# Kernel optimization log

Measured on AMD Instinct MI355X. Metric: run time of the kernel, lower is better.

The kernel has to match this reference:

```python
import jax, jax.numpy as jnp
import numpy as np

B, X_DIM, Z_DIM, K = 16384, 784, 64, 64
LOG2PI = 1.8378770664093453


def setup_inputs() -> dict:
    key = jax.random.key(0)
    ks = jax.random.split(key, 8)
    pi_raw = jax.random.uniform(ks[1], (B, K), dtype=jnp.float32) + 1e-3
    pi = pi_raw / jnp.sum(pi_raw, axis=1, keepdims=True)
    return {
        "x": jax.random.normal(ks[0], (B, X_DIM), dtype=jnp.float32),
        "pi": pi,
        "qz_mu": jax.random.normal(ks[2], (B, Z_DIM), dtype=jnp.float32),
        "qz_logsigma": 0.5 * jax.random.normal(ks[3], (B, Z_DIM), dtype=jnp.float32),
        "eps": jax.random.normal(ks[4], (B, Z_DIM), dtype=jnp.float32),
        "pz_y_mu": jax.random.normal(ks[5], (K, Z_DIM), dtype=jnp.float32),
        "pz_y_logsigma": jnp.zeros((K, Z_DIM), dtype=jnp.float32),  # log(init_sigma=1.0)
        "W_dec": jax.random.normal(ks[6], (Z_DIM, X_DIM), dtype=jnp.float32) / np.sqrt(Z_DIM),
        "b_dec": jnp.zeros((X_DIM,), dtype=jnp.float32),
    }


def reference(x, pi, qz_mu, qz_logsigma, eps, pz_y_mu, pz_y_logsigma, W_dec, b_dec):
    # GMMVAE.elbo with num_samples=1; rsample reparameterized with fixed eps.
    qs = jnp.exp(qz_logsigma)                      # [B, z]
    z = qz_mu + qs * eps                           # [B, z]

    # log p(x | z): unit-variance Gaussian likelihood with linear decoder
    mean = z @ W_dec + b_dec                       # [B, x]
    log_px_z = jnp.sum(-0.5 * (x - mean) ** 2 - 0.5 * LOG2PI)

    # py_z: vectorized over all k components (fuses the original Python loop)
    ps = jnp.exp(pz_y_logsigma)                    # [k, z]
    diff = z[:, None, :] - pz_y_mu[None, :, :]     # [B, k, z]
    comp_lp = jnp.sum(-0.5 * (diff / ps[None]) ** 2 - pz_y_logsigma[None] - 0.5 * LOG2PI, axis=-1)  # [B, k]
    log_pi = jnp.log(pi)
    pzy = comp_lp + log_pi                         # [B, k]
    log_py_z = pzy - jax.scipy.special.logsumexp(pzy, axis=1, keepdims=True)
    probs = jnp.exp(log_py_z)                      # [B, k]

    # kl_y = sum_b KL(Cat(py_z) || Cat(pi))
    kl_y = jnp.sum(probs * (log_py_z - log_pi))

    # kl_z = sum_b sum_k probs[b,k] * KL(N(qz_mu, qs) || N(mu_k, ps_k)).sum(z)
    mdiff = qz_mu[:, None, :] - pz_y_mu[None, :, :]  # [B, k, z]
    klz_bk = jnp.sum(
        pz_y_logsigma[None] - qz_logsigma[:, None, :]
        + (qs[:, None, :] ** 2 + mdiff ** 2) / (2.0 * ps[None] ** 2)
        - 0.5,
        axis=-1,
    )                                              # [B, k]
    kl_z = jnp.sum(probs * klz_bk)

    elbo = (log_px_z - kl_y - kl_z) / x.shape[0]
    return elbo
```

## Files before the change

kernel.cpp:

```cpp
#include <hip/hip_runtime.h>

#define NB 16384
#define XD 784
#define ZD 64
#define KK 64
#define LOG2PI_F 1.8378770664093453f

typedef __attribute__((ext_vector_type(8))) short short8;
typedef __attribute__((ext_vector_type(4))) float floatx4;


__device__ __forceinline__ float wave_sum(float x) {
    #pragma unroll
    for (int o = 32; o > 0; o >>= 1) x += __shfl_xor(x, o, 64);
    return x;
}

__device__ __forceinline__ unsigned short f2bf(float f) {
    unsigned u = __float_as_uint(f);
    unsigned r = (u + 0x7FFF + ((u >> 16) & 1)) >> 16;
    return (unsigned short)r;
}

__device__ __forceinline__ unsigned int pack2(float a, float b) {
    return (unsigned int)f2bf(a) | ((unsigned int)f2bf(b) << 16);
}

__device__ __forceinline__ short8 pack8(const float* v) {
    short8 r;
    unsigned int* p = (unsigned int*)&r;
    p[0] = pack2(v[0], v[1]);
    p[1] = pack2(v[2], v[3]);
    p[2] = pack2(v[4], v[5]);
    p[3] = pack2(v[6], v[7]);
    return r;
}

__global__ __launch_bounds__(256) void prep_kernel(
    const float* __restrict__ W, const float* __restrict__ pmu_g,
    const float* __restrict__ plog_g, unsigned short* __restrict__ Wt,
    unsigned short* __restrict__ Bi2, unsigned short* __restrict__ Bm1,
    float* __restrict__ Sk, float* __restrict__ Gk)
{
    const int tid = threadIdx.x;
    if (blockIdx.x < 196) {
        int idx = blockIdx.x * 256 + tid;
        int k = idx / XD;
        int n = idx - k * XD;
        Wt[n * ZD + k] = f2bf(W[idx]);
        return;
    }
    const int k  = tid >> 2;
    const int q  = tid & 3;
    const int v0 = q * 16;
    float s = 0.f, g = 0.f;
    unsigned int* pi2 = (unsigned int*)&Bi2[k * 64 + v0];
    unsigned int* pm1 = (unsigned int*)&Bm1[k * 64 + v0];
    #pragma unroll
    for (int i = 0; i < 4; ++i) {
        float4 mu4 = *(const float4*)&pmu_g[k * 64 + v0 + 4 * i];
        float4 lg4 = *(const float4*)&plog_g[k * 64 + v0 + 4 * i];
        float m0[4] = {mu4.x, mu4.y, mu4.z, mu4.w};
        float l0[4] = {lg4.x, lg4.y, lg4.z, lg4.w};
        float i2v[4], m1v[4];
        #pragma unroll
        for (int j = 0; j < 4; ++j) {
            float i2 = 0.5f * __expf(-2.f * l0[j]);
            i2v[j] = i2;
            m1v[j] = m0[j] * i2;
            g = fmaf(m0[j] * m0[j], i2, g);
            s += l0[j];
        }
        pi2[i * 2 + 0] = pack2(i2v[0], i2v[1]);
        pi2[i * 2 + 1] = pack2(i2v[2], i2v[3]);
        pm1[i * 2 + 0] = pack2(m1v[0], m1v[1]);
        pm1[i * 2 + 1] = pack2(m1v[2], m1v[3]);
    }
    s += __shfl_xor(s, 1, 64);
    s += __shfl_xor(s, 2, 64);
    g += __shfl_xor(g, 1, 64);
    g += __shfl_xor(g, 2, 64);
    if (q == 0) { Sk[k] = s; Gk[k] = g; }
}

__global__ __launch_bounds__(256) void fused_kernel(
    const float* __restrict__ x, const float* __restrict__ pi,
    const float* __restrict__ qmu, const float* __restrict__ qls,
    const float* __restrict__ eps,
    const unsigned short* __restrict__ Bi2, const unsigned short* __restrict__ Bm1,
    const float* __restrict__ Sk, const float* __restrict__ Gk,
    const unsigned short* __restrict__ Wt, const float* __restrict__ bd,
    float* __restrict__ dec_p, float* __restrict__ kly_p, float* __restrict__ klz_p)
{
    const int tid   = threadIdx.x;
    const int lane  = tid & 63;
    const int wid   = tid >> 6;
    const int mm    = lane & 15;
    const int quad  = lane >> 4;
    const int row0  = blockIdx.x * 16;
    const int arow  = row0 + mm;
    const int v0    = quad * 8;
    const int v1    = 32 + quad * 8;

    float mu[16], ls[16], ep[16];
    *(float4*)&mu[0]  = *(const float4*)&qmu[arow * 64 + v0];
    *(float4*)&mu[4]  = *(const float4*)&qmu[arow * 64 + v0 + 4];
    *(float4*)&mu[8]  = *(const float4*)&qmu[arow * 64 + v1];
    *(float4*)&mu[12] = *(const float4*)&qmu[arow * 64 + v1 + 4];
    *(float4*)&ls[0]  = *(const float4*)&qls[arow * 64 + v0];
    *(float4*)&ls[4]  = *(const float4*)&qls[arow * 64 + v0 + 4];
    *(float4*)&ls[8]  = *(const float4*)&qls[arow * 64 + v1];
    *(float4*)&ls[12] = *(const float4*)&qls[arow * 64 + v1 + 4];
    *(float4*)&ep[0]  = *(const float4*)&eps[arow * 64 + v0];
    *(float4*)&ep[4]  = *(const float4*)&eps[arow * 64 + v0 + 4];
    *(float4*)&ep[8]  = *(const float4*)&eps[arow * 64 + v1];
    *(float4*)&ep[12] = *(const float4*)&eps[arow * 64 + v1 + 4];

    float zf[16], ls_sum = 0.f;
    float qsv[16];
    #pragma unroll
    for (int j = 0; j < 16; ++j) {
        qsv[j] = __expf(ls[j]);
        zf[j]  = fmaf(qsv[j], ep[j], mu[j]);
        ls_sum += ls[j];
    }
    const short8 af0 = pack8(&zf[0]), af1 = pack8(&zf[8]);

    if (wid == 3) {
        float zz[16], zm[16], q2[16], qm[16];
        #pragma unroll
        for (int j = 0; j < 16; ++j) {
            zz[j] = zf[j] * zf[j];
            zm[j] = -2.f * zf[j];
            q2[j] = fmaf(mu[j], mu[j], qsv[j] * qsv[j]);
            qm[j] = -2.f * mu[j];
        }
        float sls = ls_sum;
        sls += __shfl_xor(sls, 16, 64);
        sls += __shfl_xor(sls, 32, 64);

        const short8 az2_0 = pack8(&zz[0]), az2_1 = pack8(&zz[8]);
        const short8 azm_0 = pack8(&zm[0]), azm_1 = pack8(&zm[8]);
        const short8 aq2_0 = pack8(&q2[0]), aq2_1 = pack8(&q2[8]);
        const short8 aqm_0 = pack8(&qm[0]), aqm_1 = pack8(&qm[8]);

        short8 bi[4][2], bm[4][2];
        float skv[4], gkv[4];
        #pragma unroll
        for (int t = 0; t < 4; ++t) {
            const int kc = t * 16 + mm;
            bi[t][0] = *(const short8*)&Bi2[kc * 64 + v0];
            bi[t][1] = *(const short8*)&Bi2[kc * 64 + v1];
            bm[t][0] = *(const short8*)&Bm1[kc * 64 + v0];
            bm[t][1] = *(const short8*)&Bm1[kc * 64 + v1];
            skv[t] = Sk[kc];
            gkv[t] = Gk[kc];
        }
        float pv[4][4];
        #pragma unroll
        for (int t = 0; t < 4; ++t)
            #pragma unroll
            for (int r = 0; r < 4; ++r)
                pv[t][r] = pi[(row0 + quad * 4 + r) * 64 + t * 16 + mm];

        floatx4 acc_a[4], acc_c[4];
        #pragma unroll
        for (int t = 0; t < 4; ++t) {
            floatx4 ca = {0.f, 0.f, 0.f, 0.f};
            ca = __builtin_amdgcn_mfma_f32_16x16x32_bf16(az2_0, bi[t][0], ca, 0, 0, 0);
            ca = __builtin_amdgcn_mfma_f32_16x16x32_bf16(az2_1, bi[t][1], ca, 0, 0, 0);
            ca = __builtin_amdgcn_mfma_f32_16x16x32_bf16(azm_0, bm[t][0], ca, 0, 0, 0);
            ca = __builtin_amdgcn_mfma_f32_16x16x32_bf16(azm_1, bm[t][1], ca, 0, 0, 0);
            acc_a[t] = ca;
            floatx4 cc = {0.f, 0.f, 0.f, 0.f};
            cc = __builtin_amdgcn_mfma_f32_16x16x32_bf16(aq2_0, bi[t][0], cc, 0, 0, 0);
            cc = __builtin_amdgcn_mfma_f32_16x16x32_bf16(aq2_1, bi[t][1], cc, 0, 0, 0);
            cc = __builtin_amdgcn_mfma_f32_16x16x32_bf16(aqm_0, bm[t][0], cc, 0, 0, 0);
            cc = __builtin_amdgcn_mfma_f32_16x16x32_bf16(aqm_1, bm[t][1], cc, 0, 0, 0);
            acc_c[t] = cc;
        }

        float comp[4][4], pz[4][4];
        #pragma unroll
        for (int t = 0; t < 4; ++t) {
            const float ck = -skv[t] - 32.0f * LOG2PI_F;
            #pragma unroll
            for (int r = 0; r < 4; ++r) {
                comp[t][r] = ck - (acc_a[t][r] + gkv[t]);
                pz[t][r] = comp[t][r] + __logf(pv[t][r]);
            }
        }

        float kly = 0.f, klz = 0.f;
        #pragma unroll
        for (int r = 0; r < 4; ++r) {
            float mx = fmaxf(fmaxf(pz[0][r], pz[1][r]), fmaxf(pz[2][r], pz[3][r]));
            #pragma unroll
            for (int o = 1; o <= 8; o <<= 1) mx = fmaxf(mx, __shfl_xor(mx, o, 64));
            float e[4];
            float s = 0.f;
            #pragma unroll
            for (int t = 0; t < 4; ++t) { e[t] = __expf(pz[t][r] - mx); s += e[t]; }
            #pragma unroll
            for (int o = 1; o <= 8; o <<= 1) s += __shfl_xor(s, o, 64);
            const float lse = mx + __logf(s);
            const float inv = __frcp_rn(s);
            const float sqr = __shfl(sls, quad * 4 + r, 64);
            #pragma unroll
            for (int t = 0; t < 4; ++t) {
                const float p = e[t] * inv;
                kly = fmaf(p, comp[t][r] - lse, kly);
                klz = fmaf(p, skv[t] - sqr + acc_c[t][r] + gkv[t] - 32.0f, klz);
            }
        }

        kly = wave_sum(kly);
        klz = wave_sum(klz);
        if (lane == 0) {
            kly_p[blockIdx.x] = kly;
            klz_p[blockIdx.x] = klz;
        }
    }

    const int xrow = (row0 + quad * 4) * XD;
    float xa0, xa1, xa2, xa3, bb;
    short8 w0, w1;
    {
        const int col = wid * 16 + mm;
        xa0 = x[xrow + 0 * XD + col];
        xa1 = x[xrow + 1 * XD + col];
        xa2 = x[xrow + 2 * XD + col];
        xa3 = x[xrow + 3 * XD + col];
        bb  = bd[col];
        w0  = *(const short8*)&Wt[col * 64 + v0];
        w1  = *(const short8*)&Wt[col * 64 + v1];
    }

    float accl = 0.f;
    #pragma unroll 1
    for (int t = wid; t < 49; t += 4) {
        const float cx0 = xa0, cx1 = xa1, cx2 = xa2, cx3 = xa3, cb = bb;
        const short8 cw0 = w0, cw1 = w1;
        const int tn = t + 4;
        if (tn < 49) {
            const int col = tn * 16 + mm;
            xa0 = x[xrow + 0 * XD + col];
            xa1 = x[xrow + 1 * XD + col];
            xa2 = x[xrow + 2 * XD + col];
            xa3 = x[xrow + 3 * XD + col];
            bb  = bd[col];
            w0  = *(const short8*)&Wt[col * 64 + v0];
            w1  = *(const short8*)&Wt[col * 64 + v1];
        }
        floatx4 c = {0.f, 0.f, 0.f, 0.f};
        c = __builtin_amdgcn_mfma_f32_16x16x32_bf16(af0, cw0, c, 0, 0, 0);
        c = __builtin_amdgcn_mfma_f32_16x16x32_bf16(af1, cw1, c, 0, 0, 0);
        float d0 = cx0 - (c[0] + cb);
        float d1 = cx1 - (c[1] + cb);
        float d2 = cx2 - (c[2] + cb);
        float d3 = cx3 - (c[3] + cb);
        accl = fmaf(d0, d0, accl);
        accl = fmaf(d1, d1, accl);
        accl = fmaf(d2, d2, accl);
        accl = fmaf(d3, d3, accl);
    }

    accl = wave_sum(accl);
    if (lane == 0) dec_p[blockIdx.x * 4 + wid] = -0.5f * accl;
}

__global__ __launch_bounds__(256) void finalize_kernel(
    const float* __restrict__ dec_p, const float* __restrict__ kly_p,
    const float* __restrict__ klz_p, float* __restrict__ out)
{
    __shared__ double s0[256], s1[256], s2[256];
    const int tid = threadIdx.x;
    double a0 = 0.0, a1 = 0.0, a2 = 0.0;
    #pragma unroll
    for (int i = 0; i < 16; ++i) a0 += (double)dec_p[tid + 256 * i];
    #pragma unroll
    for (int i = 0; i < 4; ++i) {
        a1 += (double)kly_p[tid + 256 * i];
        a2 += (double)klz_p[tid + 256 * i];
    }
    s0[tid] = a0; s1[tid] = a1; s2[tid] = a2;
    __syncthreads();
    #pragma unroll
    for (int off = 128; off > 0; off >>= 1) {
        if (tid < off) {
            s0[tid] += s0[tid + off];
            s1[tid] += s1[tid + off];
            s2[tid] += s2[tid + off];
        }
        __syncthreads();
    }
    if (tid == 0) {
        double lpx = s0[0] - 0.5 * 1.8378770664093453 * (double)NB * (double)XD;
        out[0] = (float)((lpx - s1[0] - s2[0]) / (double)NB);
    }
}

extern "C" void kernel_launch(void* const* d_in, const int* in_sizes, int n_in,
                              void* d_out, int out_size, void* d_ws, size_t ws_size,
                              hipStream_t stream) {
    const float* x    = (const float*)d_in[0];
    const float* pi   = (const float*)d_in[1];
    const float* qmu  = (const float*)d_in[2];
    const float* qls  = (const float*)d_in[3];
    const float* eps  = (const float*)d_in[4];
    const float* pmu  = (const float*)d_in[5];
    const float* plog = (const float*)d_in[6];
    const float* W    = (const float*)d_in[7];
    const float* bd   = (const float*)d_in[8];
    float* out = (float*)d_out;

    char* ws = (char*)d_ws;
    unsigned short* Wt  = (unsigned short*)(ws);
    unsigned short* Bi2 = (unsigned short*)(ws + 100352);
    unsigned short* Bm1 = (unsigned short*)(ws + 108544);
    float* Sk    = (float*)(ws + 116736);
    float* Gk    = (float*)(ws + 116992);
    float* dec_p = (float*)(ws + 117248);
    float* kly_p = (float*)(ws + 133632);
    float* klz_p = (float*)(ws + 137728);

    prep_kernel<<<197, 256, 0, stream>>>(W, pmu, plog, Wt, Bi2, Bm1, Sk, Gk);
    fused_kernel<<<NB / 16, 256, 0, stream>>>(x, pi, qmu, qls, eps,
                                              Bi2, Bm1, Sk, Gk, Wt, bd,
                                              dec_p, kly_p, klz_p);
    finalize_kernel<<<1, 256, 0, stream>>>(dec_p, kly_p, klz_p, out);
}
```

Measured before the change: 129.5 us.

## Expand reconstruction loss algebraically via x·W^T projection and Gram matrix

Replaces the decoder reconstruction (z@W then squared error over 784 columns) with the expansion ||x||^2 - 2(z·xW^T + x·b) + z^T(WW^T)z + 2z·Wb + ||b||^2. The per-row xW^T product is computed with MFMA across all four waves. A new prep kernel builds the bf16 Gram matrix WW^T. The KL work moves to wave 0 after a shared-memory reduction. This cancels large terms in fp32/bf16, which risks precision loss, and adds an extra launch and a barrier.

```diff
diff --git a/kernel.cpp b/kernel.cpp
--- a/kernel.cpp
+++ b/kernel.cpp
@@ -36,72 +36,176 @@
     return r;
 }
 
-__global__ __launch_bounds__(256) void prep_kernel(
+__device__ __forceinline__ float d4(float4 a, float4 b) {
+    return a.x * b.x + a.y * b.y + a.z * b.z + a.w * b.w;
+}
+
+__global__ __launch_bounds__(256) void prep1_kernel(
     const float* __restrict__ W, const float* __restrict__ pmu_g,
-    const float* __restrict__ plog_g, unsigned short* __restrict__ Wt,
+    const float* __restrict__ plog_g, const float* __restrict__ bd,
+    unsigned short* __restrict__ Wb16,
     unsigned short* __restrict__ Bi2, unsigned short* __restrict__ Bm1,
-    float* __restrict__ Sk, float* __restrict__ Gk)
+    float* __restrict__ Sk, float* __restrict__ Gk,
+    float* __restrict__ Wbv, float* __restrict__ sb2)
 {
     const int tid = threadIdx.x;
-    if (blockIdx.x < 196) {
+    if (blockIdx.x < 200) {
         int idx = blockIdx.x * 256 + tid;
-        int k = idx / XD;
-        int n = idx - k * XD;
-        Wt[n * ZD + k] = f2bf(W[idx]);
+        int v = idx / 800, c = idx - v * 800;
+        Wb16[idx] = (c < XD) ? f2bf(W[v * XD + c]) : (unsigned short)0;
         return;
     }
-    const int k  = tid >> 2;
-    const int q  = tid & 3;
-    const int v0 = q * 16;
-    float s = 0.f, g = 0.f;
-    unsigned int* pi2 = (unsigned int*)&Bi2[k * 64 + v0];
-    unsigned int* pm1 = (unsigned int*)&Bm1[k * 64 + v0];
-    #pragma unroll
-    for (int i = 0; i < 4; ++i) {
-        float4 mu4 = *(const float4*)&pmu_g[k * 64 + v0 + 4 * i];
-        float4 lg4 = *(const float4*)&plog_g[k * 64 + v0 + 4 * i];
-        float m0[4] = {mu4.x, mu4.y, mu4.z, mu4.w};
-        float l0[4] = {lg4.x, lg4.y, lg4.z, lg4.w};
-        float i2v[4], m1v[4];
-        #pragma unroll
-        for (int j = 0; j < 4; ++j) {
-            float i2 = 0.5f * __expf(-2.f * l0[j]);
-            i2v[j] = i2;
-            m1v[j] = m0[j] * i2;
-            g = fmaf(m0[j] * m0[j], i2, g);
-            s += l0[j];
-        }
-        pi2[i * 2 + 0] = pack2(i2v[0], i2v[1]);
-        pi2[i * 2 + 1] = pack2(i2v[2], i2v[3]);
-        pm1[i * 2 + 0] = pack2(m1v[0], m1v[1]);
-        pm1[i * 2 + 1] = pack2(m1v[2], m1v[3]);
-    }
-    s += __shfl_xor(s, 1, 64);
-    s += __shfl_xor(s, 2, 64);
-    g += __shfl_xor(g, 1, 64);
-    g += __shfl_xor(g, 2, 64);
-    if (q == 0) { Sk[k] = s; Gk[k] = g; }
-}
-
-__global__ __launch_bounds__(256) void fused_kernel(
+    if (blockIdx.x == 200) {
+        const int k  = tid >> 2;
+        const int q  = tid & 3;
+        const int v0 = q * 16;
+        float s = 0.f, g = 0.f;
+        unsigned int* pi2 = (unsigned int*)&Bi2[k * 64 + v0];
+        unsigned int* pm1 = (unsigned int*)&Bm1[k * 64 + v0];
+        #pragma unroll
+        for (int i = 0; i < 4; ++i) {
+            float4 mu4 = *(const float4*)&pmu_g[k * 64 + v0 + 4 * i];
+            float4 lg4 = *(const float4*)&plog_g[k * 64 + v0 + 4 * i];
+            float m0[4] = {mu4.x, mu4.y, mu4.z, mu4.w};
+            float l0[4] = {lg4.x, lg4.y, lg4.z, lg4.w};
+            float i2v[4], m1v[4];
+            #pragma unroll
+            for (int j = 0; j < 4; ++j) {
+                float i2 = 0.5f * __expf(-2.f * l0[j]);
+                i2v[j] = i2;
+                m1v[j] = m0[j] * i2;
+                g = fmaf(m0[j] * m0[j], i2, g);
+                s += l0[j];
+            }
+            pi2[i * 2 + 0] = pack2(i2v[0], i2v[1]);
+            pi2[i * 2 + 1] = pack2(i2v[2], i2v[3]);
+            pm1[i * 2 + 0] = pack2(m1v[0], m1v[1]);
+            pm1[i * 2 + 1] = pack2(m1v[2], m1v[3]);
+        }
+        s += __shfl_xor(s, 1, 64);
+        s += __shfl_xor(s, 2, 64);
+        g += __shfl_xor(g, 1, 64);
+        g += __shfl_xor(g, 2, 64);
+        if (q == 0) { Sk[k] = s; Gk[k] = g; }
+        return;
+    }
+    __shared__ float wl[256], bl[256];
+    const int v = tid & 63, p = tid >> 6;
+    float s = 0.f;
+    for (int j = p * 196; j < p * 196 + 196; ++j)
+        s = fmaf(W[v * XD + j], bd[j], s);
+    wl[tid] = s;
+    float b2 = 0.f;
+    for (int j = tid; j < XD; j += 256) b2 = fmaf(bd[j], bd[j], b2);
+    bl[tid] = b2;
+    __syncthreads();
+    if (tid < 64) Wbv[tid] = wl[tid] + wl[64 + tid] + wl[128 + tid] + wl[192 + tid];
+    if (tid < 32) {
+        float t2 = 0.f;
+        for (int i = tid; i < 256; i += 32) t2 += bl[i];
+        #pragma unroll
+        for (int o = 16; o > 0; o >>= 1) t2 += __shfl_xor(t2, o, 64);
+        if (tid == 0) sb2[0] = t2;
+    }
+}
+
+__global__ __launch_bounds__(64) void prep2_kernel(
+    const unsigned short* __restrict__ Wb16, unsigned short* __restrict__ G2)
+{
+    const int lane = threadIdx.x & 63;
+    const int mm = lane & 15, q = lane >> 4;
+    const int ti = blockIdx.x >> 2, tj = blockIdx.x & 3;
+    floatx4 acc = {0.f, 0.f, 0.f, 0.f};
+    #pragma unroll 5
+    for (int kt = 0; kt < 25; ++kt) {
+        const int kc = kt * 32 + q * 8;
+        short8 a = *(const short8*)&Wb16[(ti * 16 + mm) * 800 + kc];
+        short8 b = *(const short8*)&Wb16[(tj * 16 + mm) * 800 + kc];
+        acc = __builtin_amdgcn_mfma_f32_16x16x32_bf16(a, b, acc, 0, 0, 0);
+    }
+    #pragma unroll
+    for (int r = 0; r < 4; ++r)
+        G2[(ti * 16 + q * 4 + r) * 64 + tj * 16 + mm] = f2bf(acc[r]);
+}
+
+__global__ __launch_bounds__(256) void mega_kernel(
     const float* __restrict__ x, const float* __restrict__ pi,
     const float* __restrict__ qmu, const float* __restrict__ qls,
-    const float* __restrict__ eps,
+    const float* __restrict__ eps, const float* __restrict__ bd,
+    const unsigned short* __restrict__ Wb16, const unsigned short* __restrict__ G2,
     const unsigned short* __restrict__ Bi2, const unsigned short* __restrict__ Bm1,
     const float* __restrict__ Sk, const float* __restrict__ Gk,
-    const unsigned short* __restrict__ Wt, const float* __restrict__ bd,
+    const float* __restrict__ Wbv, const float* __restrict__ sb2p,
     float* __restrict__ dec_p, float* __restrict__ kly_p, float* __restrict__ klz_p)
 {
-    const int tid   = threadIdx.x;
-    const int lane  = tid & 63;
-    const int wid   = tid >> 6;
-    const int mm    = lane & 15;
-    const int quad  = lane >> 4;
-    const int row0  = blockIdx.x * 16;
-    const int arow  = row0 + mm;
-    const int v0    = quad * 8;
-    const int v1    = 32 + quad * 8;
-
+    __shared__ float XWp[4][16][64];
+    __shared__ float sxp[4][16], xbp[4][16];
+    __shared__ float us[16][64];
+
+    const int tid  = threadIdx.x;
+    const int lane = tid & 63;
+    const int wid  = tid >> 6;
+    const int mm   = lane & 15;
+    const int q    = lane >> 4;
+    const int row0 = blockIdx.x * 16;
+
+    const float* xrow = x + (row0 + mm) * XD;
+    const int tbase = wid * 6;
+    float sx2 = 0.f, xb = 0.f;
+    short8 axf[6];
+    #pragma unroll
+    for (int i = 0; i < 6; ++i) {
+        const int c = (tbase + i) * 32 + q * 8;
+        float4 a0 = *(const float4*)&xrow[c];
+        float4 a1 = *(const float4*)&xrow[c + 4];
+        float4 b0 = *(const float4*)&bd[c];
+        float4 b1 = *(const float4*)&bd[c + 4];
+        sx2 += d4(a0, a0) + d4(a1, a1);
+        xb  += d4(a0, b0) + d4(a1, b1);
+        float tmp[8] = {a0.x, a0.y, a0.z, a0.w, a1.x, a1.y, a1.z, a1.w};
+        axf[i] = pack8(tmp);
+    }
+    floatx4 acc[4] = {{0.f,0.f,0.f,0.f},{0.f,0.f,0.f,0.f},{0.f,0.f,0.f,0.f},{0.f,0.f,0.f,0.f}};
+    #pragma unroll
+    for (int i = 0; i < 6; ++i) {
+        const int kc = (tbase + i) * 32 + q * 8;
+        #pragma unroll
+        for (int t = 0; t < 4; ++t) {
+            short8 bfr = *(const short8*)&Wb16[(t * 16 + mm) * 800 + kc];
+            acc[t] = __builtin_amdgcn_mfma_f32_16x16x32_bf16(axf[i], bfr, acc[t], 0, 0, 0);
+        }
+    }
+    if (wid == 3) {
+        const int c = 768 + q * 8;
+        const bool ok = q < 2;
+        float4 z4 = {0.f, 0.f, 0.f, 0.f};
+        float4 a0 = ok ? *(const float4*)&xrow[c]     : z4;
+        float4 a1 = ok ? *(const float4*)&xrow[c + 4] : z4;
+        float4 b0 = ok ? *(const float4*)&bd[c]       : z4;
+        float4 b1 = ok ? *(const float4*)&bd[c + 4]   : z4;
+        sx2 += d4(a0, a0) + d4(a1, a1);
+        xb  += d4(a0, b0) + d4(a1, b1);
+        float tmp[8] = {a0.x, a0.y, a0.z, a0.w, a1.x, a1.y, a1.z, a1.w};
+        short8 a7 = pack8(tmp);
+        #pragma unroll
+        for (int t = 0; t < 4; ++t) {
+            short8 bfr = *(const short8*)&Wb16[(t * 16 + mm) * 800 + c];
+            acc[t] = __builtin_amdgcn_mfma_f32_16x16x32_bf16(a7, bfr, acc[t], 0, 0, 0);
+        }
+    }
+    sx2 += __shfl_xor(sx2, 16, 64); sx2 += __shfl_xor(sx2, 32, 64);
+    xb  += __shfl_xor(xb, 16, 64);  xb  += __shfl_xor(xb, 32, 64);
+    #pragma unroll
+    for (int t = 0; t < 4; ++t)
+        #pragma unroll
+        for (int r = 0; r < 4; ++r)
+            XWp[wid][q * 4 + r][t * 16 + mm] = acc[t][r];
+    if (q == 0) { sxp[wid][mm] = sx2; xbp[wid][mm] = xb; }
+    __syncthreads();
+    if (wid != 0) return;
+
+    const int arow = row0 + mm;
+    const int v0 = q * 8, v1 = 32 + q * 8;
     float mu[16], ls[16], ep[16];
     *(float4*)&mu[0]  = *(const float4*)&qmu[arow * 64 + v0];
     *(float4*)&mu[4]  = *(const float4*)&qmu[arow * 64 + v0 + 4];
@@ -116,8 +220,7 @@
     *(float4*)&ep[8]  = *(const float4*)&eps[arow * 64 + v1];
     *(float4*)&ep[12] = *(const float4*)&eps[arow * 64 + v1 + 4];
 
-    float zf[16], ls_sum = 0.f;
-    float qsv[16];
+    float zf[16], qsv[16], ls_sum = 0.f;
     #pragma unroll
     for (int j = 0; j < 16; ++j) {
         qsv[j] = __expf(ls[j]);
@@ -126,147 +229,134 @@
     }
     const short8 af0 = pack8(&zf[0]), af1 = pack8(&zf[8]);
 
-    if (wid == 3) {
-        float zz[16], zm[16], q2[16], qm[16];
-        #pragma unroll
-        for (int j = 0; j < 16; ++j) {
-            zz[j] = zf[j] * zf[j];
-            zm[j] = -2.f * zf[j];
-            q2[j] = fmaf(mu[j], mu[j], qsv[j] * qsv[j]);
-            qm[j] = -2.f * mu[j];
-        }
-        float sls = ls_sum;
-        sls += __shfl_xor(sls, 16, 64);
-        sls += __shfl_xor(sls, 32, 64);
-
-        const short8 az2_0 = pack8(&zz[0]), az2_1 = pack8(&zz[8]);
-        const short8 azm_0 = pack8(&zm[0]), azm_1 = pack8(&zm[8]);
-        const short8 aq2_0 = pack8(&q2[0]), aq2_1 = pack8(&q2[8]);
-        const short8 aqm_0 = pack8(&qm[0]), aqm_1 = pack8(&qm[8]);
-
-        short8 bi[4][2], bm[4][2];
-        float skv[4], gkv[4];
+    float zxw = 0.f, zwb = 0.f;
+    #pragma unroll
+    for (int c2 = 0; c2 < 2; ++c2) {
+        const int vb = c2 ? v1 : v0;
+        #pragma unroll
+        for (int j = 0; j < 8; ++j) {
+            float xwv = XWp[0][mm][vb + j] + XWp[1][mm][vb + j]
+                      + XWp[2][mm][vb + j] + XWp[3][mm][vb + j];
+            zxw = fmaf(zf[c2 * 8 + j], xwv, zxw);
+        }
+        float4 wb0 = *(const float4*)&Wbv[vb];
+        float4 wb1 = *(const float4*)&Wbv[vb + 4];
+        zwb += zf[c2*8+0]*wb0.x + zf[c2*8+1]*wb0.y + zf[c2*8+2]*wb0.z + zf[c2*8+3]*wb0.w
+             + zf[c2*8+4]*wb1.x + zf[c2*8+5]*wb1.y + zf[c2*8+6]*wb1.z + zf[c2*8+7]*wb1.w;
+    }
+    zxw += __shfl_xor(zxw, 16, 64); zxw += __shfl_xor(zxw, 32, 64);
+    zwb += __shfl_xor(zwb, 16, 64); zwb += __shfl_xor(zwb, 32, 64);
+    const float sxrow = sxp[0][mm] + sxp[1][mm] + sxp[2][mm] + sxp[3][mm];
+    const float xbrow = xbp[0][mm] + xbp[1][mm] + xbp[2][mm] + xbp[3][mm];
+
+    {
+        floatx4 u[4] = {{0.f,0.f,0.f,0.f},{0.f,0.f,0.f,0.f},{0.f,0.f,0.f,0.f},{0.f,0.f,0.f,0.f}};
         #pragma unroll
         for (int t = 0; t < 4; ++t) {
-            const int kc = t * 16 + mm;
-            bi[t][0] = *(const short8*)&Bi2[kc * 64 + v0];
-            bi[t][1] = *(const short8*)&Bi2[kc * 64 + v1];
-            bm[t][0] = *(const short8*)&Bm1[kc * 64 + v0];
-            bm[t][1] = *(const short8*)&Bm1[kc * 64 + v1];
-            skv[t] = Sk[kc];
-            gkv[t] = Gk[kc];
-        }
-        float pv[4][4];
+            short8 g0 = *(const short8*)&G2[(t * 16 + mm) * 64 + v0];
+            short8 g1 = *(const short8*)&G2[(t * 16 + mm) * 64 + v1];
+            u[t] = __builtin_amdgcn_mfma_f32_16x16x32_bf16(af0, g0, u[t], 0, 0, 0);
+            u[t] = __builtin_amdgcn_mfma_f32_16x16x32_bf16(af1, g1, u[t], 0, 0, 0);
+        }
         #pragma unroll
         for (int t = 0; t < 4; ++t)
             #pragma unroll
             for (int r = 0; r < 4; ++r)
-                pv[t][r] = pi[(row0 + quad * 4 + r) * 64 + t * 16 + mm];
-
-        floatx4 acc_a[4], acc_c[4];
+                us[q * 4 + r][t * 16 + mm] = u[t][r];
+    }
+    float zg2 = 0.f;
+    #pragma unroll
+    for (int j = 0; j < 8; ++j) {
+        zg2 = fmaf(zf[j],     us[mm][v0 + j], zg2);
+        zg2 = fmaf(zf[8 + j], us[mm][v1 + j], zg2);
+    }
+    zg2 += __shfl_xor(zg2, 16, 64); zg2 += __shfl_xor(zg2, 32, 64);
+
+    float zz[16], zm[16], q2[16], qm[16];
+    #pragma unroll
+    for (int j = 0; j < 16; ++j) {
+        zz[j] = zf[j] * zf[j];
+        zm[j] = -2.f * zf[j];
+        q2[j] = fmaf(mu[j], mu[j], qsv[j] * qsv[j]);
+        qm[j] = -2.f * mu[j];
+    }
+    float sls = ls_sum;
+    sls += __shfl_xor(sls, 16, 64); sls += __shfl_xor(sls, 32, 64);
+
+    const short8 az2_0 = pack8(&zz[0]), az2_1 = pack8(&zz[8]);
+    const short8 azm_0 = pack8(&zm[0]), azm_1 = pack8(&zm[8]);
+    const short8 aq2_0 = pack8(&q2[0]), aq2_1 = pack8(&q2[8]);
+    const short8 aqm_0 = pack8(&qm[0]), aqm_1 = pack8(&qm[8]);
+
+    floatx4 acc_a[4], acc_c[4];
+    float skv[4], gkv[4];
+    #pragma unroll
+    for (int t = 0; t < 4; ++t) {
+        const int kc = t * 16 + mm;
+        short8 bi0 = *(const short8*)&Bi2[kc * 64 + v0];
+        short8 bi1 = *(const short8*)&Bi2[kc * 64 + v1];
+        short8 bm0 = *(const short8*)&Bm1[kc * 64 + v0];
+        short8 bm1 = *(const short8*)&Bm1[kc * 64 + v1];
+        skv[t] = Sk[kc];
+        gkv[t] = Gk[kc];
+        floatx4 ca = {0.f, 0.f, 0.f, 0.f};
+        ca = __builtin_amdgcn_mfma_f32_16x16x32_bf16(az2_0, bi0, ca, 0, 0, 0);
+        ca = __builtin_amdgcn_mfma_f32_16x16x32_bf16(az2_1, bi1, ca, 0, 0, 0);
+        ca = __builtin_amdgcn_mfma_f32_16x16x32_bf16(azm_0, bm0, ca, 0, 0, 0);
+        ca = __builtin_amdgcn_mfma_f32_16x16x32_bf16(azm_1, bm1, ca, 0, 0, 0);
+        acc_a[t] = ca;
+        floatx4 cc = {0.f, 0.f, 0.f, 0.f};
+        cc = __builtin_amdgcn_mfma_f32_16x16x32_bf16(aq2_0, bi0, cc, 0, 0, 0);
+        cc = __builtin_amdgcn_mfma_f32_16x16x32_bf16(aq2_1, bi1, cc, 0, 0, 0);
+        cc = __builtin_amdgcn_mfma_f32_16x16x32_bf16(aqm_0, bm0, cc, 0, 0, 0);
+        cc = __builtin_amdgcn_mfma_f32_16x16x32_bf16(aqm_1, bm1, cc, 0, 0, 0);
+        acc_c[t] = cc;
+    }
+
+    float comp[4][4], pz[4][4];
+    #pragma unroll
+    for (int t = 0; t < 4; ++t) {
+        const float ck = -skv[t] - 32.0f * LOG2PI_F;
+        #pragma unroll
+        for (int r = 0; r < 4; ++r) {
+            comp[t][r] = ck - (acc_a[t][r] + gkv[t]);
+            pz[t][r] = comp[t][r] + __logf(pi[(row0 + q * 4 + r) * 64 + t * 16 + mm]);
+        }
+    }
+
+    float kly = 0.f, klz = 0.f;
+    #pragma unroll
+    for (int r = 0; r < 4; ++r) {
+        float mx = fmaxf(fmaxf(pz[0][r], pz[1][r]), fmaxf(pz[2][r], pz[3][r]));
+        #pragma unroll
+        for (int o = 1; o <= 8; o <<= 1) mx = fmaxf(mx, __shfl_xor(mx, o, 64));
+        float e[4];
+        float s = 0.f;
+        #pragma unroll
+        for (int t = 0; t < 4; ++t) { e[t] = __expf(pz[t][r] - mx); s += e[t]; }
+        #pragma unroll
+        for (int o = 1; o <= 8; o <<= 1) s += __shfl_xor(s, o, 64);
+        const float lse = mx + __logf(s);
+        const float inv = __frcp_rn(s);
+        const float sqr = __shfl(sls, q * 4 + r, 64);
         #pragma unroll
         for (int t = 0; t < 4; ++t) {
-            floatx4 ca = {0.f, 0.f, 0.f, 0.f};
-            ca = __builtin_amdgcn_mfma_f32_16x16x32_bf16(az2_0, bi[t][0], ca, 0, 0, 0);
-            ca = __builtin_amdgcn_mfma_f32_16x16x32_bf16(az2_1, bi[t][1], ca, 0, 0, 0);
-            ca = __builtin_amdgcn_mfma_f32_16x16x32_bf16(azm_0, bm[t][0], ca, 0, 0, 0);
-            ca = __builtin_amdgcn_mfma_f32_16x16x32_bf16(azm_1, bm[t][1], ca, 0, 0, 0);
-            acc_a[t] = ca;
-            floatx4 cc = {0.f, 0.f, 0.f, 0.f};
-            cc = __builtin_amdgcn_mfma_f32_16x16x32_bf16(aq2_0, bi[t][0], cc, 0, 0, 0);
-            cc = __builtin_amdgcn_mfma_f32_16x16x32_bf16(aq2_1, bi[t][1], cc, 0, 0, 0);
-            cc = __builtin_amdgcn_mfma_f32_16x16x32_bf16(aqm_0, bm[t][0], cc, 0, 0, 0);
-            cc = __builtin_amdgcn_mfma_f32_16x16x32_bf16(aqm_1, bm[t][1], cc, 0, 0, 0);
-            acc_c[t] = cc;
-        }
-
-        float comp[4][4], pz[4][4];
-        #pragma unroll
-        for (int t = 0; t < 4; ++t) {
-            const float ck = -skv[t] - 32.0f * LOG2PI_F;
-            #pragma unroll
-            for (int r = 0; r < 4; ++r) {
-                comp[t][r] = ck - (acc_a[t][r] + gkv[t]);
-                pz[t][r] = comp[t][r] + __logf(pv[t][r]);
-            }
-        }
-
-        float kly = 0.f, klz = 0.f;
-        #pragma unroll
-        for (int r = 0; r < 4; ++r) {
-            float mx = fmaxf(fmaxf(pz[0][r], pz[1][r]), fmaxf(pz[2][r], pz[3][r]));
-            #pragma unroll
-            for (int o = 1; o <= 8; o <<= 1) mx = fmaxf(mx, __shfl_xor(mx, o, 64));
-            float e[4];
-            float s = 0.f;
-            #pragma unroll
-            for (int t = 0; t < 4; ++t) { e[t] = __expf(pz[t][r] - mx); s += e[t]; }
-            #pragma unroll
-            for (int o = 1; o <= 8; o <<= 1) s += __shfl_xor(s, o, 64);
-            const float lse = mx + __logf(s);
-            const float inv = __frcp_rn(s);
-            const float sqr = __shfl(sls, quad * 4 + r, 64);
-            #pragma unroll
-            for (int t = 0; t < 4; ++t) {
-                const float p = e[t] * inv;
-                kly = fmaf(p, comp[t][r] - lse, kly);
-                klz = fmaf(p, skv[t] - sqr + acc_c[t][r] + gkv[t] - 32.0f, klz);
-            }
-        }
-
-        kly = wave_sum(kly);
-        klz = wave_sum(klz);
-        if (lane == 0) {
-            kly_p[blockIdx.x] = kly;
-            klz_p[blockIdx.x] = klz;
-        }
-    }
-
-    const int xrow = (row0 + quad * 4) * XD;
-    float xa0, xa1, xa2, xa3, bb;
-    short8 w0, w1;
-    {
-        const int col = wid * 16 + mm;
-        xa0 = x[xrow + 0 * XD + col];
-        xa1 = x[xrow + 1 * XD + col];
-        xa2 = x[xrow + 2 * XD + col];
-        xa3 = x[xrow + 3 * XD + col];
-        bb  = bd[col];
-        w0  = *(const short8*)&Wt[col * 64 + v0];
-        w1  = *(const short8*)&Wt[col * 64 + v1];
-    }
-
-    float accl = 0.f;
-    #pragma unroll 1
-    for (int t = wid; t < 49; t += 4) {
-        const float cx0 = xa0, cx1 = xa1, cx2 = xa2, cx3 = xa3, cb = bb;
-        const short8 cw0 = w0, cw1 = w1;
-        const int tn = t + 4;
-        if (tn < 49) {
-            const int col = tn * 16 + mm;
-            xa0 = x[xrow + 0 * XD + col];
-            xa1 = x[xrow + 1 * XD + col];
-            xa2 = x[xrow + 2 * XD + col];
-            xa3 = x[xrow + 3 * XD + col];
-            bb  = bd[col];
-            w0  = *(const short8*)&Wt[col * 64 + v0];
-            w1  = *(const short8*)&Wt[col * 64 + v1];
-        }
-        floatx4 c = {0.f, 0.f, 0.f, 0.f};
-        c = __builtin_amdgcn_mfma_f32_16x16x32_bf16(af0, cw0, c, 0, 0, 0);
-        c = __builtin_amdgcn_mfma_f32_16x16x32_bf16(af1, cw1, c, 0, 0, 0);
-        float d0 = cx0 - (c[0] + cb);
-        float d1 = cx1 - (c[1] + cb);
-        float d2 = cx2 - (c[2] + cb);
-        float d3 = cx3 - (c[3] + cb);
-        accl = fmaf(d0, d0, accl);
-        accl = fmaf(d1, d1, accl);
-        accl = fmaf(d2, d2, accl);
-        accl = fmaf(d3, d3, accl);
-    }
-
-    accl = wave_sum(accl);
-    if (lane == 0) dec_p[blockIdx.x * 4 + wid] = -0.5f * accl;
+            const float p = e[t] * inv;
+            kly = fmaf(p, comp[t][r] - lse, kly);
+            klz = fmaf(p, skv[t] - sqr + acc_c[t][r] + gkv[t] - 32.0f, klz);
+        }
+    }
+
+    const float dec_row = sxrow - 2.f * (zxw + xbrow) + zg2 + 2.f * zwb + sb2p[0];
+    float dsum = (q == 0) ? dec_row : 0.f;
+    dsum = wave_sum(dsum);
+    kly = wave_sum(kly);
+    klz = wave_sum(klz);
+    if (lane == 0) {
+        dec_p[blockIdx.x] = -0.5f * dsum;
+        kly_p[blockIdx.x] = kly;
+        klz_p[blockIdx.x] = klz;
+    }
 }
 
 __global__ __launch_bounds__(256) void finalize_kernel(
@@ -277,9 +367,8 @@
     const int tid = threadIdx.x;
     double a0 = 0.0, a1 = 0.0, a2 = 0.0;
     #pragma unroll
-    for (int i = 0; i < 16; ++i) a0 += (double)dec_p[tid + 256 * i];
-    #pragma unroll
     for (int i = 0; i < 4; ++i) {
+        a0 += (double)dec_p[tid + 256 * i];
         a1 += (double)kly_p[tid + 256 * i];
         a2 += (double)klz_p[tid + 256 * i];
     }
@@ -315,18 +404,22 @@
     float* out = (float*)d_out;
 
     char* ws = (char*)d_ws;
-    unsigned short* Wt  = (unsigned short*)(ws);
-    unsigned short* Bi2 = (unsigned short*)(ws + 100352);
-    unsigned short* Bm1 = (unsigned short*)(ws + 108544);
-    float* Sk    = (float*)(ws + 116736);
-    float* Gk    = (float*)(ws + 116992);
-    float* dec_p = (float*)(ws + 117248);
-    float* kly_p = (float*)(ws + 133632);
-    float* klz_p = (float*)(ws + 137728);
-
-    prep_kernel<<<197, 256, 0, stream>>>(W, pmu, plog, Wt, Bi2, Bm1, Sk, Gk);
-    fused_kernel<<<NB / 16, 256, 0, stream>>>(x, pi, qmu, qls, eps,
-                                              Bi2, Bm1, Sk, Gk, Wt, bd,
-                                              dec_p, kly_p, klz_p);
+    unsigned short* Wb16 = (unsigned short*)(ws);
+    unsigned short* G2   = (unsigned short*)(ws + 102400);
+    unsigned short* Bi2  = (unsigned short*)(ws + 110592);
+    unsigned short* Bm1  = (unsigned short*)(ws + 118784);
+    float* Sk    = (float*)(ws + 126976);
+    float* Gk    = (float*)(ws + 127232);
+    float* Wbv   = (float*)(ws + 127488);
+    float* sb2   = (float*)(ws + 127744);
+    float* dec_p = (float*)(ws + 127808);
+    float* kly_p = (float*)(ws + 131904);
+    float* klz_p = (float*)(ws + 136000);
+
+    prep1_kernel<<<202, 256, 0, stream>>>(W, pmu, plog, bd, Wb16, Bi2, Bm1, Sk, Gk, Wbv, sb2);
+    prep2_kernel<<<16, 64, 0, stream>>>(Wb16, G2);
+    mega_kernel<<<NB / 16, 256, 0, stream>>>(x, pi, qmu, qls, eps, bd,
+                                             Wb16, G2, Bi2, Bm1, Sk, Gk, Wbv, sb2,
+                                             dec_p, kly_p, klz_p);
     finalize_kernel<<<1, 256, 0, stream>>>(dec_p, kly_p, klz_p, out);
 }
```

Measured after the change: 137.2 us. 1.06x slower.
